# Kernel tuning notes

Hardware: AMD Instinct MI355X
Metric: run time of the kernel (lower is better)

The kernel has to match this reference:

```python
import jax, jax.numpy as jnp
import numpy as np

BN_EPS = 1e-5
OUT_H, OUT_W = 32, 32  # crop_size / output_stride = 512/16


def setup_inputs() -> dict:
    key = jax.random.key(0)
    k1, k2, k3, k4 = jax.random.split(key, 4)
    x = jax.random.normal(k1, (16, 2048, 32, 32), dtype=jnp.float32)
    # conv1x1 weight, bias-free: [dim_out, dim_in]
    W = jax.random.normal(k2, (256, 2048), dtype=jnp.float32) * (1.0 / np.sqrt(2048.0))
    gamma = jax.random.normal(k3, (256,), dtype=jnp.float32) * 0.1 + 1.0
    beta = jax.random.normal(k4, (256,), dtype=jnp.float32) * 0.1
    return {"x": x, "W": W, "gamma": gamma, "beta": beta}


def reference(x, W, gamma, beta):
    # 1x1 conv, no bias: channel contraction
    y = jnp.einsum("nchw,oc->nohw", x, W)  # [N, dim_out, H, W]
    # BatchNorm2d in training mode: batch statistics over (N, H, W), biased var
    mean = jnp.mean(y, axis=(0, 2, 3), keepdims=True)
    var = jnp.mean(jnp.square(y - mean), axis=(0, 2, 3), keepdims=True)
    g = gamma.reshape(1, -1, 1, 1)
    b = beta.reshape(1, -1, 1, 1)
    y = g * (y - mean) * jax.lax.rsqrt(var + BN_EPS) + b
    # global average pool to 1x1
    pooled = jnp.mean(y, axis=(2, 3), keepdims=True)  # [N, dim_out, 1, 1]
    # adaptive avg pool from 1x1 to (OUT_H, OUT_W) is a pure broadcast
    out = jnp.broadcast_to(pooled, pooled.shape[:2] + (OUT_H, OUT_W))
    return out
```

## Files before the change

kernel.cpp:

```cpp
#include <hip/hip_runtime.h>
#include <hip/hip_bf16.h>
#include <stdint.h>

#define NB   16
#define CIN  2048
#define OUTC 256
#define HW   1024
#define BJ   64
#define BK   64
#define NJT  (HW / BJ)
#define KSTEPS (CIN / BK)

typedef __attribute__((ext_vector_type(8))) short bf16x8;
typedef __attribute__((ext_vector_type(4))) float f32x4;
typedef __attribute__((ext_vector_type(4))) unsigned int u32x4;

__device__ __forceinline__ unsigned int f2bf(float f) {
    union { float f; unsigned int u; } a; a.f = f;
    return (a.u + 0x7FFFu + ((a.u >> 16) & 1u)) >> 16;
}

__device__ __forceinline__ void block_sync_lds() {
    asm volatile("s_waitcnt lgkmcnt(0)" ::: "memory");
    __builtin_amdgcn_s_barrier();
    asm volatile("" ::: "memory");
}

__global__ void wprep_kernel(const float* __restrict__ W, unsigned short* __restrict__ Afrag) {
    int g  = blockIdx.x * blockDim.x + threadIdx.x;
    int o  = g >> 8;
    int kc = g & 255;
    const float4* p = reinterpret_cast<const float4*>(W + o * CIN + kc * 8);
    float4 v0 = p[0], v1 = p[1];
    u32x4 pk;
    pk.x = f2bf(v0.x) | (f2bf(v0.y) << 16);
    pk.y = f2bf(v0.z) | (f2bf(v0.w) << 16);
    pk.z = f2bf(v1.x) | (f2bf(v1.y) << 16);
    pk.w = f2bf(v1.z) | (f2bf(v1.w) << 16);
    int ks32 = kc >> 2, g8 = kc & 3;
    int lane = g8 * 16 + (o & 15), ot = o >> 4;
    *reinterpret_cast<u32x4*>(Afrag + (((size_t)ks32 * 16 + ot) * 64 + lane) * 8) = pk;
}

__global__ __launch_bounds__(512, 2) void gemm_stats_kernel(
    const float* __restrict__ x,
    const unsigned short* __restrict__ Afrag,
    float* __restrict__ s1_part,
    float* __restrict__ s2_part)
{
    __shared__ __align__(16) unsigned short B0[4096], B1[4096];

    const int tid  = threadIdx.x;
    const int lane = tid & 63;
    const int wave = tid >> 6;
    const int blk  = blockIdx.x;
    const int n    = blk >> 4;
    const int jt   = blk & 15;
    const int j0   = jt * BJ;

    const float* xn = x + (size_t)n * CIN * HW;

    const int bj = tid & 63;
    const int kh = tid >> 6;
    const float* Bgp = xn + (size_t)(kh * 8) * HW + j0 + bj;
    const int offB = (kh >> 2) * 2048 + (bj >> 4) * 512 + (kh & 3) * 128 + (bj & 15) * 8;

    const int rbase = lane * 8;

    const unsigned short* Ab = Afrag + (size_t)lane * 8;

#define LDA(ks, R) { _Pragma("unroll") \
    for (int h = 0; h < 2; ++h) _Pragma("unroll") for (int t = 0; t < 2; ++t) \
        R[h * 2 + t] = *(const u32x4*)(Ab + ((((ks) * 2 + h) * 16 + 2 * wave + t) * 64) * 8); }
#define LDB(ks, F) { const float* p = Bgp + (size_t)(ks) * BK * HW; \
    _Pragma("unroll") for (int i = 0; i < 8; ++i) F[i] = p[(size_t)i * HW]; }
#define WRITEB(Bb, F) { u32x4 pk; \
    pk.x = f2bf(F[0]) | (f2bf(F[1]) << 16); pk.y = f2bf(F[2]) | (f2bf(F[3]) << 16); \
    pk.z = f2bf(F[4]) | (f2bf(F[5]) << 16); pk.w = f2bf(F[6]) | (f2bf(F[7]) << 16); \
    *(u32x4*)&Bb[offB] = pk; }
#define COMPUTE(Bb, R) { _Pragma("unroll") \
    for (int h = 0; h < 2; ++h) { \
        bf16x8 af0 = *(const bf16x8*)&R[h * 2 + 0]; \
        bf16x8 af1 = *(const bf16x8*)&R[h * 2 + 1]; \
        _Pragma("unroll") \
        for (int ni = 0; ni < 4; ++ni) { \
            bf16x8 bf = *(const bf16x8*)&Bb[h * 2048 + ni * 512 + rbase]; \
            acc[0][ni] = __builtin_amdgcn_mfma_f32_16x16x32_bf16(af0, bf, acc[0][ni], 0, 0, 0); \
            acc[1][ni] = __builtin_amdgcn_mfma_f32_16x16x32_bf16(af1, bf, acc[1][ni], 0, 0, 0); \
    } } }

    f32x4 acc[2][4] = {};
    u32x4 Aa0[4], Aa1[4];
    float Bs0[8], Bs1[8];

    LDA(0, Aa0); LDB(0, Bs0);
    LDA(1, Aa1); LDB(1, Bs1);
    WRITEB(B0, Bs0);
    LDB(2, Bs0);
    block_sync_lds();

    #pragma unroll 1
    for (int ks = 0; ks < KSTEPS; ks += 2) {
        COMPUTE(B0, Aa0);
        {
            int ka = (ks + 2 < KSTEPS) ? ks + 2 : KSTEPS - 1;
            LDA(ka, Aa0);
            WRITEB(B1, Bs1);
            int kb = (ks + 3 < KSTEPS) ? ks + 3 : KSTEPS - 1;
            LDB(kb, Bs1);
            block_sync_lds();
        }
        COMPUTE(B1, Aa1);
        {
            int ka = (ks + 3 < KSTEPS) ? ks + 3 : KSTEPS - 1;
            LDA(ka, Aa1);
        }
        if (ks + 2 < KSTEPS) {
            WRITEB(B0, Bs0);
            int kb = (ks + 4 < KSTEPS) ? ks + 4 : KSTEPS - 1;
            LDB(kb, Bs0);
            block_sync_lds();
        }
    }

    float rs[2][4], rq[2][4];
    #pragma unroll
    for (int mi = 0; mi < 2; ++mi) {
        #pragma unroll
        for (int r = 0; r < 4; ++r) {
            float s = 0.f, q = 0.f;
            #pragma unroll
            for (int ni = 0; ni < 4; ++ni) {
                float v = acc[mi][ni][r];
                s += v; q += v * v;
            }
            rs[mi][r] = s; rq[mi][r] = q;
        }
    }
    #pragma unroll
    for (int m = 1; m < 16; m <<= 1) {
        #pragma unroll
        for (int mi = 0; mi < 2; ++mi) {
            #pragma unroll
            for (int r = 0; r < 4; ++r) {
                rs[mi][r] += __shfl_xor(rs[mi][r], m, 64);
                rq[mi][r] += __shfl_xor(rq[mi][r], m, 64);
            }
        }
    }
    const int rA = lane & 15;
    if (rA == 0) {
        const int gK = lane >> 4;
        #pragma unroll
        for (int mi = 0; mi < 2; ++mi) {
            #pragma unroll
            for (int r = 0; r < 4; ++r) {
                int o = wave * 32 + mi * 16 + gK * 4 + r;
                s1_part[(jt * NB + n) * OUTC + o] = rs[mi][r];
                s2_part[blk * OUTC + o]           = rq[mi][r];
            }
        }
    }
#undef LDA
#undef LDB
#undef WRITEB
#undef COMPUTE
}

__global__ __launch_bounds__(256) void finalize_bcast_kernel(
    const float* __restrict__ s1_part,
    const float* __restrict__ s2_part,
    const float* __restrict__ gamma,
    const float* __restrict__ beta,
    float* __restrict__ out)
{
    const int tid   = threadIdx.x;
    const int slice = tid & 15;
    const int o_l   = tid >> 4;
    const int n0    = blockIdx.x >> 4;
    const int o     = (blockIdx.x & 15) * 16 + o_l;

    float S1 = 0.f, S2 = 0.f;
    #pragma unroll
    for (int q = 0; q < 16; ++q) {
        int p = slice * 16 + q;
        S1 += s1_part[p * OUTC + o];
        S2 += s2_part[p * OUTC + o];
    }
    float s1n = s1_part[(slice * NB + n0) * OUTC + o];
    #pragma unroll
    for (int m = 1; m < 16; m <<= 1) {
        S1  += __shfl_xor(S1, m, 64);
        S2  += __shfl_xor(S2, m, 64);
        s1n += __shfl_xor(s1n, m, 64);
    }
    float mean = S1 * (1.f / 16384.f);
    float var  = S2 * (1.f / 16384.f) - mean * mean;
    float inv  = rsqrtf(var + 1e-5f);
    float v = gamma[o] * (s1n * (1.f / 1024.f) - mean) * inv + beta[o];

    float4 vv = make_float4(v, v, v, v);
    float4* dst = reinterpret_cast<float4*>(out + ((size_t)(n0 * OUTC + o)) * HW);
    #pragma unroll
    for (int it = 0; it < 16; ++it)
        dst[it * 16 + slice] = vv;
}

extern "C" void kernel_launch(void* const* d_in, const int* in_sizes, int n_in,
                              void* d_out, int out_size, void* d_ws, size_t ws_size,
                              hipStream_t stream) {
    const float* x     = (const float*)d_in[0];
    const float* W     = (const float*)d_in[1];
    const float* gamma = (const float*)d_in[2];
    const float* beta  = (const float*)d_in[3];
    float* out = (float*)d_out;

    char* ws = (char*)d_ws;
    unsigned short* Afrag = (unsigned short*)ws;
    float* s1_part = (float*)(ws + (1 << 20));
    float* s2_part = (float*)(ws + (1 << 20) + (256 << 10));

    hipLaunchKernelGGL(wprep_kernel, dim3(256), dim3(256), 0, stream, W, Afrag);
    hipLaunchKernelGGL(gemm_stats_kernel, dim3(256), dim3(512), 0, stream,
                       x, Afrag, s1_part, s2_part);
    hipLaunchKernelGGL(finalize_bcast_kernel, dim3(NB * (OUTC / 16)), dim3(256), 0, stream,
                       s1_part, s2_part, gamma, beta, out);
}
```

Before: 48.03 us.

## Interleave B loads and MFMAs in barrier-separated phases with setprio

Splits each k-step into four phases. Each phase issues two global B loads and LDS fragment reads, then four MFMAs with raised wave priority, separated by workgroup barriers. A-fragment prefetch distance drops to one step and the loop unrolls two steps with swapped buffers. This aims to keep global loads and matrix work interleaved across waves, at the cost of several extra barriers per k-step.

After: 49.77 us. +3.6%, slower.

```diff
diff --git a/kernel.cpp b/kernel.cpp
--- a/kernel.cpp
+++ b/kernel.cpp
@@ -22,6 +22,11 @@
 
 __device__ __forceinline__ void block_sync_lds() {
     asm volatile("s_waitcnt lgkmcnt(0)" ::: "memory");
+    __builtin_amdgcn_s_barrier();
+    asm volatile("" ::: "memory");
+}
+__device__ __forceinline__ void phase_bar() {
+    asm volatile("" ::: "memory");
     __builtin_amdgcn_s_barrier();
     asm volatile("" ::: "memory");
 }
@@ -66,61 +71,68 @@
     const int offB = (kh >> 2) * 2048 + (bj >> 4) * 512 + (kh & 3) * 128 + (bj & 15) * 8;
 
     const int rbase = lane * 8;
-
     const unsigned short* Ab = Afrag + (size_t)lane * 8;
 
 #define LDA(ks, R) { _Pragma("unroll") \
     for (int h = 0; h < 2; ++h) _Pragma("unroll") for (int t = 0; t < 2; ++t) \
         R[h * 2 + t] = *(const u32x4*)(Ab + ((((ks) * 2 + h) * 16 + 2 * wave + t) * 64) * 8); }
-#define LDB(ks, F) { const float* p = Bgp + (size_t)(ks) * BK * HW; \
-    _Pragma("unroll") for (int i = 0; i < 8; ++i) F[i] = p[(size_t)i * HW]; }
+#define LDB2(ks, F, i0) { int kk = ((ks) < KSTEPS) ? (ks) : KSTEPS - 1; \
+    const float* p = Bgp + (size_t)kk * BK * HW; \
+    F[i0] = p[(size_t)(i0) * HW]; F[(i0) + 1] = p[(size_t)((i0) + 1) * HW]; }
 #define WRITEB(Bb, F) { u32x4 pk; \
     pk.x = f2bf(F[0]) | (f2bf(F[1]) << 16); pk.y = f2bf(F[2]) | (f2bf(F[3]) << 16); \
     pk.z = f2bf(F[4]) | (f2bf(F[5]) << 16); pk.w = f2bf(F[6]) | (f2bf(F[7]) << 16); \
     *(u32x4*)&Bb[offB] = pk; }
-#define COMPUTE(Bb, R) { _Pragma("unroll") \
-    for (int h = 0; h < 2; ++h) { \
-        bf16x8 af0 = *(const bf16x8*)&R[h * 2 + 0]; \
-        bf16x8 af1 = *(const bf16x8*)&R[h * 2 + 1]; \
-        _Pragma("unroll") \
-        for (int ni = 0; ni < 4; ++ni) { \
-            bf16x8 bf = *(const bf16x8*)&Bb[h * 2048 + ni * 512 + rbase]; \
-            acc[0][ni] = __builtin_amdgcn_mfma_f32_16x16x32_bf16(af0, bf, acc[0][ni], 0, 0, 0); \
-            acc[1][ni] = __builtin_amdgcn_mfma_f32_16x16x32_bf16(af1, bf, acc[1][ni], 0, 0, 0); \
-    } } }
+#define BFRAG(Bb, h, ni) (*(const bf16x8*)&Bb[(h) * 2048 + (ni) * 512 + rbase])
+#define MFMA4(R, hh, blo, bhi, ni0) { \
+    bf16x8 a0_ = *(const bf16x8*)&R[(hh) * 2 + 0]; \
+    bf16x8 a1_ = *(const bf16x8*)&R[(hh) * 2 + 1]; \
+    __builtin_amdgcn_s_setprio(1); \
+    acc[0][ni0]     = __builtin_amdgcn_mfma_f32_16x16x32_bf16(a0_, blo, acc[0][ni0], 0, 0, 0); \
+    acc[1][ni0]     = __builtin_amdgcn_mfma_f32_16x16x32_bf16(a1_, blo, acc[1][ni0], 0, 0, 0); \
+    acc[0][(ni0)+1] = __builtin_amdgcn_mfma_f32_16x16x32_bf16(a0_, bhi, acc[0][(ni0)+1], 0, 0, 0); \
+    acc[1][(ni0)+1] = __builtin_amdgcn_mfma_f32_16x16x32_bf16(a1_, bhi, acc[1][(ni0)+1], 0, 0, 0); \
+    __builtin_amdgcn_s_setprio(0); }
+
+#define STEP(tv, bufC, bufN, BsL, BsW, Acur, Aalt) { \
+     \
+    bf16x8 b0_ = BFRAG(bufC, 0, 0), b1_ = BFRAG(bufC, 0, 1); \
+    LDB2((tv) + 2, BsL, 0); \
+    LDA(((tv) + 1 < KSTEPS) ? (tv) + 1 : KSTEPS - 1, Aalt); \
+    MFMA4(Acur, 0, b0_, b1_, 0); \
+    phase_bar(); \
+     \
+    bf16x8 b2_ = BFRAG(bufC, 0, 2), b3_ = BFRAG(bufC, 0, 3); \
+    LDB2((tv) + 2, BsL, 2); \
+    MFMA4(Acur, 0, b2_, b3_, 2); \
+    phase_bar(); \
+     \
+    bf16x8 b4_ = BFRAG(bufC, 1, 0), b5_ = BFRAG(bufC, 1, 1); \
+    LDB2((tv) + 2, BsL, 4); \
+    MFMA4(Acur, 1, b4_, b5_, 0); \
+    phase_bar(); \
+     \
+    bf16x8 b6_ = BFRAG(bufC, 1, 2), b7_ = BFRAG(bufC, 1, 3); \
+    LDB2((tv) + 2, BsL, 6); \
+    if ((tv) + 1 < KSTEPS) { WRITEB(bufN, BsW); } \
+    MFMA4(Acur, 1, b6_, b7_, 2); \
+    if ((tv) + 1 < KSTEPS) { block_sync_lds(); } \
+}
 
     f32x4 acc[2][4] = {};
     u32x4 Aa0[4], Aa1[4];
-    float Bs0[8], Bs1[8];
-
-    LDA(0, Aa0); LDB(0, Bs0);
-    LDA(1, Aa1); LDB(1, Bs1);
-    WRITEB(B0, Bs0);
-    LDB(2, Bs0);
+    float BsA[8], BsB[8];
+
+    LDB2(0, BsA, 0); LDB2(0, BsA, 2); LDB2(0, BsA, 4); LDB2(0, BsA, 6);
+    LDA(0, Aa0);
+    LDB2(1, BsB, 0); LDB2(1, BsB, 2); LDB2(1, BsB, 4); LDB2(1, BsB, 6);
+    WRITEB(B0, BsA);
     block_sync_lds();
 
     #pragma unroll 1
     for (int ks = 0; ks < KSTEPS; ks += 2) {
-        COMPUTE(B0, Aa0);
-        {
-            int ka = (ks + 2 < KSTEPS) ? ks + 2 : KSTEPS - 1;
-            LDA(ka, Aa0);
-            WRITEB(B1, Bs1);
-            int kb = (ks + 3 < KSTEPS) ? ks + 3 : KSTEPS - 1;
-            LDB(kb, Bs1);
-            block_sync_lds();
-        }
-        COMPUTE(B1, Aa1);
-        {
-            int ka = (ks + 3 < KSTEPS) ? ks + 3 : KSTEPS - 1;
-            LDA(ka, Aa1);
-        }
-        if (ks + 2 < KSTEPS) {
-            WRITEB(B0, Bs0);
-            int kb = (ks + 4 < KSTEPS) ? ks + 4 : KSTEPS - 1;
-            LDB(kb, Bs0);
-            block_sync_lds();
-        }
+        STEP(ks,     B0, B1, BsA, BsB, Aa0, Aa1);
+        STEP(ks + 1, B1, B0, BsB, BsA, Aa1, Aa0);
     }
 
     float rs[2][4], rq[2][4];
@@ -148,8 +160,7 @@
             }
         }
     }
-    const int rA = lane & 15;
-    if (rA == 0) {
+    if ((lane & 15) == 0) {
         const int gK = lane >> 4;
         #pragma unroll
         for (int mi = 0; mi < 2; ++mi) {
@@ -162,9 +173,11 @@
         }
     }
 #undef LDA
-#undef LDB
+#undef LDB2
 #undef WRITEB
-#undef COMPUTE
+#undef BFRAG
+#undef MFMA4
+#undef STEP
 }
 
 __global__ __launch_bounds__(256) void finalize_bcast_kernel(
```

## Double K tile per step and restructure load/compute pipeline in GEMM

Applied to the files above, without the earlier changes.

Raises the K-tile from 64 to 128 so each LDS stage holds twice as many input channels, which halves the number of barriers and loop iterations. Each thread now loads and converts 16 fp32 values per stage, and the A-fragment registers double. The prefetch schedule is simplified to a one-stage-ahead register buffer through a STEP macro. The cost is higher register pressure and larger LDS use at two blocks per CU, and the global-load latency may be less well hidden.

Measured after the change: 51.11 us. 6.4% more time.

```diff
diff --git a/kernel.cpp b/kernel.cpp
--- a/kernel.cpp
+++ b/kernel.cpp
@@ -7,7 +7,7 @@
 #define OUTC 256
 #define HW   1024
 #define BJ   64
-#define BK   64
+#define BK   128
 #define NJT  (HW / BJ)
 #define KSTEPS (CIN / BK)
 
@@ -48,7 +48,7 @@
     float* __restrict__ s1_part,
     float* __restrict__ s2_part)
 {
-    __shared__ __align__(16) unsigned short B0[4096], B1[4096];
+    __shared__ __align__(16) unsigned short B0[8192], B1[8192];
 
     const int tid  = threadIdx.x;
     const int lane = tid & 63;
@@ -66,61 +66,54 @@
     const int offB = (kh >> 2) * 2048 + (bj >> 4) * 512 + (kh & 3) * 128 + (bj & 15) * 8;
 
     const int rbase = lane * 8;
-
     const unsigned short* Ab = Afrag + (size_t)lane * 8;
 
+#define CLMP(v) (((v) < KSTEPS) ? (v) : KSTEPS - 1)
 #define LDA(ks, R) { _Pragma("unroll") \
-    for (int h = 0; h < 2; ++h) _Pragma("unroll") for (int t = 0; t < 2; ++t) \
-        R[h * 2 + t] = *(const u32x4*)(Ab + ((((ks) * 2 + h) * 16 + 2 * wave + t) * 64) * 8); }
+    for (int c = 0; c < 4; ++c) _Pragma("unroll") for (int t = 0; t < 2; ++t) \
+        R[c * 2 + t] = *(const u32x4*)(Ab + ((((ks) * 4 + c) * 16 + 2 * wave + t) * 64) * 8); }
 #define LDB(ks, F) { const float* p = Bgp + (size_t)(ks) * BK * HW; \
-    _Pragma("unroll") for (int i = 0; i < 8; ++i) F[i] = p[(size_t)i * HW]; }
+    _Pragma("unroll") for (int i = 0; i < 8; ++i) F[i] = p[(size_t)i * HW]; \
+    _Pragma("unroll") for (int i = 0; i < 8; ++i) F[8 + i] = p[(size_t)(64 + i) * HW]; }
 #define WRITEB(Bb, F) { u32x4 pk; \
     pk.x = f2bf(F[0]) | (f2bf(F[1]) << 16); pk.y = f2bf(F[2]) | (f2bf(F[3]) << 16); \
     pk.z = f2bf(F[4]) | (f2bf(F[5]) << 16); pk.w = f2bf(F[6]) | (f2bf(F[7]) << 16); \
-    *(u32x4*)&Bb[offB] = pk; }
+    *(u32x4*)&Bb[offB] = pk; \
+    pk.x = f2bf(F[8]) | (f2bf(F[9]) << 16);  pk.y = f2bf(F[10]) | (f2bf(F[11]) << 16); \
+    pk.z = f2bf(F[12]) | (f2bf(F[13]) << 16); pk.w = f2bf(F[14]) | (f2bf(F[15]) << 16); \
+    *(u32x4*)&Bb[offB + 4096] = pk; }
 #define COMPUTE(Bb, R) { _Pragma("unroll") \
-    for (int h = 0; h < 2; ++h) { \
-        bf16x8 af0 = *(const bf16x8*)&R[h * 2 + 0]; \
-        bf16x8 af1 = *(const bf16x8*)&R[h * 2 + 1]; \
+    for (int c = 0; c < 4; ++c) { \
+        bf16x8 af0 = *(const bf16x8*)&R[c * 2 + 0]; \
+        bf16x8 af1 = *(const bf16x8*)&R[c * 2 + 1]; \
         _Pragma("unroll") \
         for (int ni = 0; ni < 4; ++ni) { \
-            bf16x8 bf = *(const bf16x8*)&Bb[h * 2048 + ni * 512 + rbase]; \
+            bf16x8 bf = *(const bf16x8*)&Bb[c * 2048 + ni * 512 + rbase]; \
             acc[0][ni] = __builtin_amdgcn_mfma_f32_16x16x32_bf16(af0, bf, acc[0][ni], 0, 0, 0); \
             acc[1][ni] = __builtin_amdgcn_mfma_f32_16x16x32_bf16(af1, bf, acc[1][ni], 0, 0, 0); \
     } } }
 
+#define STEP(tv, bufC, bufN, BsL, BsW, Acur) { \
+    COMPUTE(bufC, Acur); \
+    LDA(CLMP((tv) + 2), Acur); \
+    if ((tv) + 1 < KSTEPS) { WRITEB(bufN, BsW); } \
+    LDB(CLMP((tv) + 2), BsL); \
+    if ((tv) + 1 < KSTEPS) { block_sync_lds(); } \
+}
+
     f32x4 acc[2][4] = {};
-    u32x4 Aa0[4], Aa1[4];
-    float Bs0[8], Bs1[8];
-
-    LDA(0, Aa0); LDB(0, Bs0);
-    LDA(1, Aa1); LDB(1, Bs1);
-    WRITEB(B0, Bs0);
-    LDB(2, Bs0);
+    u32x4 Aa0[8], Aa1[8];
+    float BsA[16], BsB[16];
+
+    LDA(0, Aa0); LDB(0, BsA);
+    LDA(1, Aa1); LDB(1, BsB);
+    WRITEB(B0, BsA);
     block_sync_lds();
 
     #pragma unroll 1
     for (int ks = 0; ks < KSTEPS; ks += 2) {
-        COMPUTE(B0, Aa0);
-        {
-            int ka = (ks + 2 < KSTEPS) ? ks + 2 : KSTEPS - 1;
-            LDA(ka, Aa0);
-            WRITEB(B1, Bs1);
-            int kb = (ks + 3 < KSTEPS) ? ks + 3 : KSTEPS - 1;
-            LDB(kb, Bs1);
-            block_sync_lds();
-        }
-        COMPUTE(B1, Aa1);
-        {
-            int ka = (ks + 3 < KSTEPS) ? ks + 3 : KSTEPS - 1;
-            LDA(ka, Aa1);
-        }
-        if (ks + 2 < KSTEPS) {
-            WRITEB(B0, Bs0);
-            int kb = (ks + 4 < KSTEPS) ? ks + 4 : KSTEPS - 1;
-            LDB(kb, Bs0);
-            block_sync_lds();
-        }
+        STEP(ks,     B0, B1, BsA, BsB, Aa0);
+        STEP(ks + 1, B1, B0, BsB, BsA, Aa1);
     }
 
     float rs[2][4], rq[2][4];
@@ -148,8 +141,7 @@
             }
         }
     }
-    const int rA = lane & 15;
-    if (rA == 0) {
+    if ((lane & 15) == 0) {
         const int gK = lane >> 4;
         #pragma unroll
         for (int mi = 0; mi < 2; ++mi) {
@@ -161,10 +153,12 @@
             }
         }
     }
+#undef CLMP
 #undef LDA
 #undef LDB
 #undef WRITEB
 #undef COMPUTE
+#undef STEP
 }
 
 __global__ __launch_bounds__(256) void finalize_bcast_kernel(
```

## Fuse weight prep, GEMM-stats and finalize into one kernel with grid syncs

Applied to the files above, without the earlier changes.

Merges the three kernel launches (weight bf16 packing, GEMM with BN partial statistics, finalize/broadcast) into a single persistent kernel of 256 blocks, separated by atomic-counter grid barriers. This removes the launch gaps and inter-kernel drains between stages. The GEMM main loop now keeps four x-prefetch register sets in flight instead of two, deepening the global-load pipeline. In exchange it adds a memset per call, relies on all 256 blocks being co-resident for the spin barriers, and uses more registers.

New measurement: 94.07 us. 95.9% more time.

```diff
diff --git a/kernel.cpp b/kernel.cpp
--- a/kernel.cpp
+++ b/kernel.cpp
@@ -10,6 +10,7 @@
 #define BK   64
 #define NJT  (HW / BJ)
 #define KSTEPS (CIN / BK)
+#define NBLK 256
 
 typedef __attribute__((ext_vector_type(8))) short bf16x8;
 typedef __attribute__((ext_vector_type(4))) float f32x4;
@@ -26,30 +27,29 @@
     asm volatile("" ::: "memory");
 }
 
-__global__ void wprep_kernel(const float* __restrict__ W, unsigned short* __restrict__ Afrag) {
-    int g  = blockIdx.x * blockDim.x + threadIdx.x;
-    int o  = g >> 8;
-    int kc = g & 255;
-    const float4* p = reinterpret_cast<const float4*>(W + o * CIN + kc * 8);
-    float4 v0 = p[0], v1 = p[1];
-    u32x4 pk;
-    pk.x = f2bf(v0.x) | (f2bf(v0.y) << 16);
-    pk.y = f2bf(v0.z) | (f2bf(v0.w) << 16);
-    pk.z = f2bf(v1.x) | (f2bf(v1.y) << 16);
-    pk.w = f2bf(v1.z) | (f2bf(v1.w) << 16);
-    int ks32 = kc >> 2, g8 = kc & 3;
-    int lane = g8 * 16 + (o & 15), ot = o >> 4;
-    *reinterpret_cast<u32x4*>(Afrag + (((size_t)ks32 * 16 + ot) * 64 + lane) * 8) = pk;
-}
-
-__global__ __launch_bounds__(512, 2) void gemm_stats_kernel(
+__device__ __forceinline__ void grid_sync(unsigned int* cnt) {
+    __syncthreads();
+    if (threadIdx.x == 0) {
+        __threadfence();
+        atomicAdd(cnt, 1u);
+        while (__hip_atomic_load(cnt, __ATOMIC_RELAXED, __HIP_MEMORY_SCOPE_AGENT) < NBLK)
+            __builtin_amdgcn_s_sleep(2);
+        __threadfence();
+    }
+    __syncthreads();
+}
+
+__global__ __launch_bounds__(512, 2) void fused_kernel(
     const float* __restrict__ x,
-    const unsigned short* __restrict__ Afrag,
-    float* __restrict__ s1_part,
-    float* __restrict__ s2_part)
+    const float* __restrict__ W,
+    const float* __restrict__ gamma,
+    const float* __restrict__ beta,
+    float* __restrict__ out,
+    unsigned short* Afrag,
+    float* s1_part,
+    float* s2_part,
+    unsigned int* syncnt)
 {
-    __shared__ __align__(16) unsigned short B0[4096], B1[4096];
-
     const int tid  = threadIdx.x;
     const int lane = tid & 63;
     const int wave = tid >> 6;
@@ -58,17 +58,35 @@
     const int jt   = blk & 15;
     const int j0   = jt * BJ;
 
-    const float* xn = x + (size_t)n * CIN * HW;
-
-    const int bj = tid & 63;
-    const int kh = tid >> 6;
-    const float* Bgp = xn + (size_t)(kh * 8) * HW + j0 + bj;
-    const int offB = (kh >> 2) * 2048 + (bj >> 4) * 512 + (kh & 3) * 128 + (bj & 15) * 8;
-
-    const int rbase = lane * 8;
-
-    const unsigned short* Ab = Afrag + (size_t)lane * 8;
-
+    if (tid < 256) {
+        int g  = blk * 256 + tid;
+        int o  = g >> 8;
+        int kc = g & 255;
+        const float4* p = reinterpret_cast<const float4*>(W + o * CIN + kc * 8);
+        float4 v0 = p[0], v1 = p[1];
+        u32x4 pk;
+        pk.x = f2bf(v0.x) | (f2bf(v0.y) << 16);
+        pk.y = f2bf(v0.z) | (f2bf(v0.w) << 16);
+        pk.z = f2bf(v1.x) | (f2bf(v1.y) << 16);
+        pk.w = f2bf(v1.z) | (f2bf(v1.w) << 16);
+        int ks32 = kc >> 2, g8 = kc & 3;
+        int l = g8 * 16 + (o & 15), ot = o >> 4;
+        *reinterpret_cast<u32x4*>(Afrag + (((size_t)ks32 * 16 + ot) * 64 + l) * 8) = pk;
+    }
+    grid_sync(&syncnt[0]);
+
+    {
+        __shared__ __align__(16) unsigned short B0[4096], B1[4096];
+
+        const float* xn = x + (size_t)n * CIN * HW;
+        const int bj = tid & 63;
+        const int kh = tid >> 6;
+        const float* Bgp = xn + (size_t)(kh * 8) * HW + j0 + bj;
+        const int offB = (kh >> 2) * 2048 + (bj >> 4) * 512 + (kh & 3) * 128 + (bj & 15) * 8;
+        const int rbase = lane * 8;
+        const unsigned short* Ab = Afrag + (size_t)lane * 8;
+
+#define CLMP(v) (((v) < KSTEPS) ? (v) : KSTEPS - 1)
 #define LDA(ks, R) { _Pragma("unroll") \
     for (int h = 0; h < 2; ++h) _Pragma("unroll") for (int t = 0; t < 2; ++t) \
         R[h * 2 + t] = *(const u32x4*)(Ab + ((((ks) * 2 + h) * 16 + 2 * wave + t) * 64) * 8); }
@@ -89,121 +107,100 @@
             acc[1][ni] = __builtin_amdgcn_mfma_f32_16x16x32_bf16(af1, bf, acc[1][ni], 0, 0, 0); \
     } } }
 
-    f32x4 acc[2][4] = {};
-    u32x4 Aa0[4], Aa1[4];
-    float Bs0[8], Bs1[8];
-
-    LDA(0, Aa0); LDB(0, Bs0);
-    LDA(1, Aa1); LDB(1, Bs1);
-    WRITEB(B0, Bs0);
-    LDB(2, Bs0);
-    block_sync_lds();
-
-    #pragma unroll 1
-    for (int ks = 0; ks < KSTEPS; ks += 2) {
-        COMPUTE(B0, Aa0);
-        {
-            int ka = (ks + 2 < KSTEPS) ? ks + 2 : KSTEPS - 1;
-            LDA(ka, Aa0);
-            WRITEB(B1, Bs1);
-            int kb = (ks + 3 < KSTEPS) ? ks + 3 : KSTEPS - 1;
-            LDB(kb, Bs1);
-            block_sync_lds();
-        }
-        COMPUTE(B1, Aa1);
-        {
-            int ka = (ks + 3 < KSTEPS) ? ks + 3 : KSTEPS - 1;
-            LDA(ka, Aa1);
-        }
-        if (ks + 2 < KSTEPS) {
-            WRITEB(B0, Bs0);
-            int kb = (ks + 4 < KSTEPS) ? ks + 4 : KSTEPS - 1;
-            LDB(kb, Bs0);
-            block_sync_lds();
-        }
-    }
-
-    float rs[2][4], rq[2][4];
-    #pragma unroll
-    for (int mi = 0; mi < 2; ++mi) {
-        #pragma unroll
-        for (int r = 0; r < 4; ++r) {
-            float s = 0.f, q = 0.f;
-            #pragma unroll
-            for (int ni = 0; ni < 4; ++ni) {
-                float v = acc[mi][ni][r];
-                s += v; q += v * v;
+        f32x4 acc[2][4] = {};
+        u32x4 Aa0[4], Aa1[4];
+        float S0r[8], S1r[8], S2r[8], S3r[8];
+
+        LDB(0, S0r); LDB(1, S1r); LDB(2, S2r); LDB(3, S3r);
+        LDA(0, Aa0); LDA(1, Aa1);
+        WRITEB(B0, S0r);
+        block_sync_lds();
+
+        #pragma unroll 1
+        for (int ks = 0; ks < KSTEPS; ks += 4) {
+            COMPUTE(B0, Aa0); LDA(CLMP(ks + 2), Aa0);
+            WRITEB(B1, S1r); LDB(CLMP(ks + 4), S0r); block_sync_lds();
+            COMPUTE(B1, Aa1); LDA(CLMP(ks + 3), Aa1);
+            WRITEB(B0, S2r); LDB(CLMP(ks + 5), S1r); block_sync_lds();
+            COMPUTE(B0, Aa0); LDA(CLMP(ks + 4), Aa0);
+            WRITEB(B1, S3r); LDB(CLMP(ks + 6), S2r); block_sync_lds();
+            COMPUTE(B1, Aa1); LDA(CLMP(ks + 5), Aa1);
+            if (ks + 4 < KSTEPS) {
+                WRITEB(B0, S0r); LDB(CLMP(ks + 7), S3r); block_sync_lds();
             }
-            rs[mi][r] = s; rq[mi][r] = q;
-        }
-    }
-    #pragma unroll
-    for (int m = 1; m < 16; m <<= 1) {
-        #pragma unroll
-        for (int mi = 0; mi < 2; ++mi) {
+        }
+
+        float rs[2][4], rq[2][4];
+        #pragma unroll
+        for (int mi = 0; mi < 2; ++mi)
             #pragma unroll
             for (int r = 0; r < 4; ++r) {
-                rs[mi][r] += __shfl_xor(rs[mi][r], m, 64);
-                rq[mi][r] += __shfl_xor(rq[mi][r], m, 64);
+                float s = 0.f, q = 0.f;
+                #pragma unroll
+                for (int ni = 0; ni < 4; ++ni) {
+                    float v = acc[mi][ni][r];
+                    s += v; q += v * v;
+                }
+                rs[mi][r] = s; rq[mi][r] = q;
             }
-        }
-    }
-    const int rA = lane & 15;
-    if (rA == 0) {
-        const int gK = lane >> 4;
-        #pragma unroll
-        for (int mi = 0; mi < 2; ++mi) {
+        #pragma unroll
+        for (int m = 1; m < 16; m <<= 1)
             #pragma unroll
-            for (int r = 0; r < 4; ++r) {
-                int o = wave * 32 + mi * 16 + gK * 4 + r;
-                s1_part[(jt * NB + n) * OUTC + o] = rs[mi][r];
-                s2_part[blk * OUTC + o]           = rq[mi][r];
-            }
-        }
-    }
+            for (int mi = 0; mi < 2; ++mi)
+                #pragma unroll
+                for (int r = 0; r < 4; ++r) {
+                    rs[mi][r] += __shfl_xor(rs[mi][r], m, 64);
+                    rq[mi][r] += __shfl_xor(rq[mi][r], m, 64);
+                }
+        if ((lane & 15) == 0) {
+            const int gK = lane >> 4;
+            #pragma unroll
+            for (int mi = 0; mi < 2; ++mi)
+                #pragma unroll
+                for (int r = 0; r < 4; ++r) {
+                    int o = wave * 32 + mi * 16 + gK * 4 + r;
+                    s1_part[(jt * NB + n) * OUTC + o] = rs[mi][r];
+                    s2_part[blk * OUTC + o]           = rq[mi][r];
+                }
+        }
+#undef CLMP
 #undef LDA
 #undef LDB
 #undef WRITEB
 #undef COMPUTE
-}
-
-__global__ __launch_bounds__(256) void finalize_bcast_kernel(
-    const float* __restrict__ s1_part,
-    const float* __restrict__ s2_part,
-    const float* __restrict__ gamma,
-    const float* __restrict__ beta,
-    float* __restrict__ out)
-{
-    const int tid   = threadIdx.x;
-    const int slice = tid & 15;
-    const int o_l   = tid >> 4;
-    const int n0    = blockIdx.x >> 4;
-    const int o     = (blockIdx.x & 15) * 16 + o_l;
-
-    float S1 = 0.f, S2 = 0.f;
-    #pragma unroll
-    for (int q = 0; q < 16; ++q) {
-        int p = slice * 16 + q;
-        S1 += s1_part[p * OUTC + o];
-        S2 += s2_part[p * OUTC + o];
-    }
-    float s1n = s1_part[(slice * NB + n0) * OUTC + o];
-    #pragma unroll
-    for (int m = 1; m < 16; m <<= 1) {
-        S1  += __shfl_xor(S1, m, 64);
-        S2  += __shfl_xor(S2, m, 64);
-        s1n += __shfl_xor(s1n, m, 64);
-    }
-    float mean = S1 * (1.f / 16384.f);
-    float var  = S2 * (1.f / 16384.f) - mean * mean;
-    float inv  = rsqrtf(var + 1e-5f);
-    float v = gamma[o] * (s1n * (1.f / 1024.f) - mean) * inv + beta[o];
-
-    float4 vv = make_float4(v, v, v, v);
-    float4* dst = reinterpret_cast<float4*>(out + ((size_t)(n0 * OUTC + o)) * HW);
-    #pragma unroll
-    for (int it = 0; it < 16; ++it)
-        dst[it * 16 + slice] = vv;
+    }
+    grid_sync(&syncnt[1]);
+
+    {
+        const int slice = tid & 31;
+        const int o     = (blk & 15) * 16 + (tid >> 5);
+        const int n0    = blk >> 4;
+
+        float S1 = 0.f, S2 = 0.f;
+        #pragma unroll
+        for (int q = 0; q < 8; ++q) {
+            int p = slice * 8 + q;
+            S1 += s1_part[p * OUTC + o];
+            S2 += s2_part[p * OUTC + o];
+        }
+        float s1n = (slice < NJT) ? s1_part[(slice * NB + n0) * OUTC + o] : 0.f;
+        #pragma unroll
+        for (int m = 1; m < 32; m <<= 1) {
+            S1  += __shfl_xor(S1, m, 64);
+            S2  += __shfl_xor(S2, m, 64);
+            s1n += __shfl_xor(s1n, m, 64);
+        }
+        float mean = S1 * (1.f / 16384.f);
+        float var  = S2 * (1.f / 16384.f) - mean * mean;
+        float inv  = rsqrtf(var + 1e-5f);
+        float v = gamma[o] * (s1n * (1.f / 1024.f) - mean) * inv + beta[o];
+
+        float4 vv = make_float4(v, v, v, v);
+        float4* dst = reinterpret_cast<float4*>(out + ((size_t)(n0 * OUTC + o)) * HW);
+        #pragma unroll
+        for (int it = 0; it < 8; ++it)
+            dst[it * 32 + slice] = vv;
+    }
 }
 
 extern "C" void kernel_launch(void* const* d_in, const int* in_sizes, int n_in,
@@ -219,10 +216,9 @@
     unsigned short* Afrag = (unsigned short*)ws;
     float* s1_part = (float*)(ws + (1 << 20));
     float* s2_part = (float*)(ws + (1 << 20) + (256 << 10));
-
-    hipLaunchKernelGGL(wprep_kernel, dim3(256), dim3(256), 0, stream, W, Afrag);
-    hipLaunchKernelGGL(gemm_stats_kernel, dim3(256), dim3(512), 0, stream,
-                       x, Afrag, s1_part, s2_part);
-    hipLaunchKernelGGL(finalize_bcast_kernel, dim3(NB * (OUTC / 16)), dim3(256), 0, stream,
-                       s1_part, s2_part, gamma, beta, out);
-}
+    unsigned int* syncnt = (unsigned int*)(ws + (1 << 20) + (512 << 10));
+
+    hipMemsetAsync(syncnt, 0, 16, stream);
+    hipLaunchKernelGGL(fused_kernel, dim3(NBLK), dim3(512), 0, stream,
+                       x, W, gamma, beta, out, Afrag, s1_part, s2_part, syncnt);
+}
```
